# Performance work log

Measured on AMD Instinct MI355X. Metric: run time of the kernel, lower is better.

## Reference

```python
import jax, jax.numpy as jnp
import numpy as np
import math

MODULE_NUM = 256
OUTPUT_DIM = 257
HID = 64          # self.hidden_dim
STEP_DIM = 16
BATCH = 1024
SOS = MODULE_NUM + 1
EOS = MODULE_NUM
MAX_LEN = MODULE_NUM


def setup_inputs() -> dict:
    key = jax.random.key(0)
    ks = jax.random.split(key, 12)
    s = 0.05
    f32 = jnp.float32
    return {
        "step": 100,
        "batch_size": BATCH,
        "token_embed": jax.random.normal(ks[0], (MODULE_NUM + 2, HID), f32) * s,
        "step_table": jax.random.normal(ks[1], (MAX_LEN + 1, STEP_DIM), f32) * s,
        "w_ih_f": jax.random.normal(ks[2], (3 * HID, HID), f32) * s,
        "w_hh_f": jax.random.normal(ks[3], (3 * HID, HID), f32) * s,
        "b_ih_f": jax.random.normal(ks[4], (3 * HID,), f32) * s,
        "b_hh_f": jax.random.normal(ks[5], (3 * HID,), f32) * s,
        "w_ih_b": jax.random.normal(ks[6], (3 * HID, HID), f32) * s,
        "w_hh_b": jax.random.normal(ks[7], (3 * HID, HID), f32) * s,
        "b_ih_b": jax.random.normal(ks[8], (3 * HID,), f32) * s,
        "b_hh_b": jax.random.normal(ks[9], (3 * HID,), f32) * s,
        "film_w": jax.random.normal(ks[10], (4 * HID, STEP_DIM), f32) * s,
        "film_b": jnp.zeros((4 * HID,), f32),
        "dec_w": jax.random.normal(ks[11], (OUTPUT_DIM, 2 * HID), f32) * s,
        "dec_b": jnp.zeros((OUTPUT_DIM,), f32),
    }


def _gru_cell(x, h, w_ih, w_hh, b_ih, b_hh):
    # PyTorch GRU cell math
    gi = x @ w_ih.T + b_ih              # [B, 3H]
    gh = h @ w_hh.T + b_hh              # [B, 3H]
    i_r, i_z, i_n = jnp.split(gi, 3, axis=-1)
    h_r, h_z, h_n = jnp.split(gh, 3, axis=-1)
    r = jax.nn.sigmoid(i_r + h_r)
    z = jax.nn.sigmoid(i_z + h_z)
    n = jnp.tanh(i_n + r * h_n)
    return (1.0 - z) * n + z * h


def reference(step, batch_size, token_embed, step_table,
              w_ih_f, w_hh_f, b_ih_f, b_hh_f,
              w_ih_b, w_hh_b, b_ih_b, b_hh_b,
              film_w, film_b, dec_w, dec_b):
    # exponential-decay temperature (host scalar, matches _exp_decay_tau)
    tau_max, tau_min, half_life = 2.5, 0.2, 3000
    decay = math.log(2.0) / max(1, half_life)
    temperature = max(1e-06, tau_min + (tau_max - tau_min) * math.exp(-decay * max(0, int(step))))
    B = int(batch_size)

    def step_fn(carry, t):
        h_f, h_b, inp, sel, done = carry
        x = token_embed[inp]                              # [B, H]
        h_f2 = _gru_cell(x, h_f, w_ih_f, w_hh_f, b_ih_f, b_hh_f)
        h_b2 = _gru_cell(x, h_b, w_ih_b, w_hh_b, b_ih_b, b_hh_b)
        hs = jnp.concatenate([h_f2, h_b2], axis=-1)       # [B, 2H]
        film = jnp.tanh(step_table[t] @ film_w.T + film_b)  # [4H]
        gamma, beta = jnp.split(film, 2)
        hs = hs * (1.0 + gamma) + beta
        logits = hs @ dec_w.T + dec_b                     # [B, V]
        masked = jnp.where(sel, -jnp.inf, logits) / temperature
        logp = jax.nn.log_softmax(masked, axis=-1)
        action = jnp.argmax(logp, axis=-1)                # greedy (is_val=True)
        lp = jnp.take_along_axis(logp, action[:, None], axis=-1)[:, 0]
        valid = ~done
        done2 = done | (action == EOS)
        sel2 = sel.at[jnp.arange(B), action].set(True)
        return (h_f2, h_b2, action.astype(jnp.int32), sel2, done2), (action.astype(jnp.int32), lp * valid, valid)

    init = (jnp.zeros((B, HID), jnp.float32),
            jnp.zeros((B, HID), jnp.float32),
            jnp.full((B,), SOS, jnp.int32),
            jnp.zeros((B, OUTPUT_DIM), bool),
            jnp.zeros((B,), bool))
    _, (actions, log_probs, valid) = jax.lax.scan(step_fn, init, jnp.arange(MAX_LEN))
    # [B, L] layout; positions after EOS are masked out via `valid`
    return actions.T, log_probs.T, valid.T
```

## Files before the change

### kernel.cpp

```cpp
#include <hip/hip_runtime.h>
#include <cmath>

typedef float v2f __attribute__((ext_vector_type(2)));

#define GI_STRIDE (258*192)
#define FILM_OFF  (2*GI_STRIDE)
#define TOTAL_PRE (FILM_OFF + 256*256)

#define B_TOT   1024
#define L_MAX   256
#define SOS_TOK 257
#define EOS_TOK 256

#define KEEPF(x) asm volatile("" : "+v"(x))

#define PK_LO(acc, w, x) asm("v_pk_fma_f32 %0, %1, %2, %0 op_sel:[0,0,0] op_sel_hi:[1,0,1]" : "+v"(acc) : "v"(w), "v"(x))
#define PK_HI(acc, w, x) asm("v_pk_fma_f32 %0, %1, %2, %0 op_sel:[0,1,0] op_sel_hi:[1,1,1]" : "+v"(acc) : "v"(w), "v"(x))

#define DPPI(old, src, ctrl, rmask) __builtin_amdgcn_update_dpp(old, src, ctrl, rmask, 0xF, false)

#define AMAX_STAGE(ctrl, rmask) do { \
    const int   _vi = __builtin_bit_cast(int, mv); \
    const float _ov = __builtin_bit_cast(float, DPPI(_vi, _vi, ctrl, rmask)); \
    const int   _oi = DPPI(mi, mi, ctrl, rmask); \
    if (_ov > mv || (_ov == mv && _oi < mi)) { mv = _ov; mi = _oi; } \
} while (0)

#define SUM_STAGE(s, ctrl, rmask) do { \
    (s) += __builtin_bit_cast(float, DPPI(0, __builtin_bit_cast(int, (s)), ctrl, rmask)); \
} while (0)

#define AMAX64() do { \
    AMAX_STAGE(0x111, 0xF); AMAX_STAGE(0x112, 0xF); \
    AMAX_STAGE(0x114, 0xF); AMAX_STAGE(0x118, 0xF); \
    AMAX_STAGE(0x142, 0xA); AMAX_STAGE(0x143, 0xC); \
} while (0)
#define SUM64(s) do { \
    SUM_STAGE(s, 0x111, 0xF); SUM_STAGE(s, 0x112, 0xF); \
    SUM_STAGE(s, 0x114, 0xF); SUM_STAGE(s, 0x118, 0xF); \
    SUM_STAGE(s, 0x142, 0xA); SUM_STAGE(s, 0x143, 0xC); \
} while (0)
#define SUM16(s) do { \
    SUM_STAGE(s, 0x111, 0xF); SUM_STAGE(s, 0x112, 0xF); \
    SUM_STAGE(s, 0x114, 0xF); SUM_STAGE(s, 0x118, 0xF); \
} while (0)

__global__ __launch_bounds__(256) void aag_precompute(
    const float* __restrict__ token_embed,
    const float* __restrict__ step_table,
    const float* __restrict__ w_ih_f, const float* __restrict__ b_ih_f,
    const float* __restrict__ w_ih_b, const float* __restrict__ b_ih_b,
    const float* __restrict__ film_w, const float* __restrict__ film_b,
    float* __restrict__ ws)
{
    int idx = blockIdx.x * 256 + threadIdx.x;
    if (idx < FILM_OFF) {
        int m     = idx / GI_STRIDE;
        int rem   = idx - m * GI_STRIDE;
        int token = rem / 192;
        int r     = rem - token * 192;
        const float* wih = (m ? w_ih_b : w_ih_f) + r * 64;
        const float* te  = token_embed + token * 64;
        float acc = (m ? b_ih_b : b_ih_f)[r];
        #pragma unroll 8
        for (int k = 0; k < 64; ++k) acc += te[k] * wih[k];
        ws[idx] = acc;
    } else if (idx < TOTAL_PRE) {
        int q  = idx - FILM_OFF;
        int tt = q >> 8, j = q & 255;
        const float* st = step_table + tt * 16;
        const float* fw = film_w + j * 16;
        float acc = film_b[j];
        #pragma unroll
        for (int s = 0; s < 16; ++s) acc += st[s] * fw[s];
        int pos = (j < 128) ? (2 * j) : (2 * (j - 128) + 1);
        ws[FILM_OFF + tt * 256 + pos] = tanhf(acc);
    }
}

__global__ __launch_bounds__(512)
__attribute__((amdgpu_waves_per_eu(1, 2)))
void aag_decode(
    const int* __restrict__ step_ptr,
    const float* __restrict__ w_hh_f, const float* __restrict__ b_hh_f,
    const float* __restrict__ w_hh_b, const float* __restrict__ b_hh_b,
    const float* __restrict__ dec_w, const float* __restrict__ dec_b,
    const float* __restrict__ ws,
    float* __restrict__ out)
{
    __shared__ __align__(16) float hbuf[2][4][64];
    __shared__ __align__(16) float ghL[2][4][192];
    __shared__ __align__(16) float hsL[4][128];
    __shared__ __align__(16) float plL[2][4][264];

    const int tid = threadIdx.x;
    const int wv  = tid >> 6;
    const int ln  = tid & 63;
    const int e   = wv >> 1;
    const int m   = wv & 1;
    const bool sduty = (wv == 0) || (wv == 3) || (wv == 5) || (wv == 6);

    float invT;
    {
        int step = step_ptr[0];
        if (step < 0) step = 0;
        double T = 0.2 + 2.3 * exp(-(0.6931471805599453 / 3000.0) * (double)step);
        if (T < 1e-6) T = 1e-6;
        invT = (float)(1.0 / T);
    }

    const bool isDec = (tid < 256);
    const bool isEos = (tid >= 256 && tid < 272);
    const bool isGru = (tid >= 320);
    const int  dh    = tid >> 7;
    const int  dq    = tid & 127;
    const int  gj    = tid - 320;
    const int  gm    = (gj >= 96) ? 1 : 0;
    const int  gp    = gj - 96 * gm;
    const int  ec    = tid - 256;

    v2f wreg[64];
    #pragma unroll
    for (int j = 0; j < 64; ++j) wreg[j] = (v2f){0.f, 0.f};
    v2f bias2 = {0.f, 0.f};
    if (isDec) {
        const float* dw = dec_w + (2 * dq) * 128 + dh * 64;
        #pragma unroll
        for (int k = 0; k < 64; ++k) wreg[k] = (v2f){dw[k], dw[128 + k]};
        if (dh == 0) bias2 = (v2f){dec_b[2 * dq], dec_b[2 * dq + 1]};
    } else if (isGru) {
        const float* whh = (gm ? w_hh_b : w_hh_f) + (2 * gp) * 64;
        #pragma unroll
        for (int k = 0; k < 64; ++k) wreg[k] = (v2f){whh[k], whh[64 + k]};
        const float* bhh = (gm ? b_hh_b : b_hh_f) + 2 * gp;
        bias2 = (v2f){bhh[0], bhh[1]};
    } else if (isEos) {
        const float* p = dec_w + 256 * 128 + ec * 8;
        #pragma unroll
        for (int k = 0; k < 4; ++k) wreg[k] = (v2f){p[2 * k], p[2 * k + 1]};
        bias2 = (v2f){dec_b[256], 0.f};
    }
    #pragma unroll
    for (int j = 0; j < 64; ++j) KEEPF(wreg[j]);
    KEEPF(bias2);

    ((float*)hbuf)[tid] = 0.f;
    if (isGru) {
        #pragma unroll
        for (int e2 = 0; e2 < 4; ++e2)
            *(v2f*)&ghL[gm][e2][2 * gp] = bias2;
    }

    bool s0m = false, s1m = false, s2m = false, s3m = false, s4m = false;
    bool done = false;

    const float* filmT = ws + FILM_OFF;
    const float* giT   = ws + m * GI_STRIDE;
    float ga, be;
    {
        const float2 f = *(const float2*)&filmT[(m * 64 + ln) * 2];
        ga = f.x; be = f.y;
    }
    float gi_r, gi_z, gi_n;
    {
        const float* gp2 = giT + SOS_TOK * 192;
        gi_r = gp2[ln]; gi_z = gp2[64 + ln]; gi_n = gp2[128 + ln];
    }

    const int b0 = blockIdx.x * 4;
    float* __restrict__ out_act = out;
    float* __restrict__ out_lp  = out + B_TOT * L_MAX;
    float* __restrict__ out_val = out + 2 * B_TOT * L_MAX;

    __syncthreads();

    for (int t = 0; t <= L_MAX; ++t) {
        #pragma unroll
        for (int j = 0; j < 64; ++j) KEEPF(wreg[j]);

        float hr = 0.f, hz = 0.f, hn = 0.f, hp = 0.f;
        if (t < L_MAX) {
            hr = ghL[m][e][ln];
            hz = ghL[m][e][64 + ln];
            hn = ghL[m][e][128 + ln];
            hp = hbuf[m][e][ln];
        }
        if (t > 0) {
            const float u0 = plL[0][e][ln]       + plL[1][e][ln];
            const float u1 = plL[0][e][64 + ln]  + plL[1][e][64 + ln];
            const float u2 = plL[0][e][128 + ln] + plL[1][e][128 + ln];
            const float u3 = plL[0][e][192 + ln] + plL[1][e][192 + ln];
            float mv = s0m ? -INFINITY : u0;
            int   mi = ln;
            { const float v = s1m ? -INFINITY : u1; if (v > mv) { mv = v; mi = 64 + ln; } }
            { const float v = s2m ? -INFINITY : u2; if (v > mv) { mv = v; mi = 128 + ln; } }
            { const float v = s3m ? -INFINITY : u3; if (v > mv) { mv = v; mi = 192 + ln; } }
            float u4 = 0.f;
            if (ln == 0) {
                u4 = plL[0][e][256];
                const float v = s4m ? -INFINITY : u4;
                if (v > mv) { mv = v; mi = 256; }
            }
            AMAX64();
            const int   a   = __builtin_amdgcn_readlane(mi, 63);
            const float mvU = __builtin_bit_cast(float,
                                __builtin_amdgcn_readlane(__builtin_bit_cast(int, mv), 63));
            {
                const float* gp2 = giT + a * 192;
                gi_r = gp2[ln]; gi_z = gp2[64 + ln]; gi_n = gp2[128 + ln];
            }
            if (sduty) {
                float S = 0.f;
                if (!s0m) S += __expf((u0 - mvU) * invT);
                if (!s1m) S += __expf((u1 - mvU) * invT);
                if (!s2m) S += __expf((u2 - mvU) * invT);
                if (!s3m) S += __expf((u3 - mvU) * invT);
                if (ln == 0 && !s4m) S += __expf((u4 - mvU) * invT);
                SUM64(S);
                const float Su = __builtin_bit_cast(float,
                                    __builtin_amdgcn_readlane(__builtin_bit_cast(int, S), 63));
                if (ln == 0) {
                    const int b = b0 + e;
                    out_act[b * L_MAX + (t - 1)] = (float)a;
                    out_lp [b * L_MAX + (t - 1)] = done ? 0.f : -__logf(Su);
                    out_val[b * L_MAX + (t - 1)] = done ? 0.f : 1.f;
                }
            }
            if (a == EOS_TOK) done = true;
            if ((a & 63) == ln) {
                if (a < 64) s0m = true; else if (a < 128) s1m = true;
                else if (a < 192) s2m = true; else if (a < 256) s3m = true;
                else s4m = true;
            }
        }
        if (t == L_MAX) break;

        {
            const float r  = 1.f / (1.f + expf(-(gi_r + hr)));
            const float z  = 1.f / (1.f + expf(-(gi_z + hz)));
            const float n  = tanhf(gi_n + r * hn);
            const float h2 = (1.f - z) * n + z * hp;
            hbuf[m][e][ln] = h2;
            hsL[e][m * 64 + ln] = h2 * (1.f + ga) + be;
        }
        __syncthreads();

        {
            const int tn = (t + 1 < L_MAX) ? t + 1 : L_MAX - 1;
            const float2 f = *(const float2*)&filmT[tn * 256 + (m * 64 + ln) * 2];
            ga = f.x; be = f.y;
        }
        if (isDec) {
            v2f a0 = bias2, a1 = bias2, a2 = bias2, a3 = bias2;
            const int hb = dh * 64;
            #pragma unroll
            for (int jj = 0; jj < 16; ++jj) {
                const float4 x0 = *(const float4*)&hsL[0][hb + 4 * jj];
                const float4 x1 = *(const float4*)&hsL[1][hb + 4 * jj];
                const float4 x2 = *(const float4*)&hsL[2][hb + 4 * jj];
                const float4 x3 = *(const float4*)&hsL[3][hb + 4 * jj];
                const v2f* x0v = (const v2f*)&x0;
                const v2f* x1v = (const v2f*)&x1;
                const v2f* x2v = (const v2f*)&x2;
                const v2f* x3v = (const v2f*)&x3;
                const v2f w0 = wreg[4*jj], w1 = wreg[4*jj+1], w2 = wreg[4*jj+2], w3 = wreg[4*jj+3];
                PK_LO(a0, w0, x0v[0]); PK_HI(a0, w1, x0v[0]);
                PK_LO(a0, w2, x0v[1]); PK_HI(a0, w3, x0v[1]);
                PK_LO(a1, w0, x1v[0]); PK_HI(a1, w1, x1v[0]);
                PK_LO(a1, w2, x1v[1]); PK_HI(a1, w3, x1v[1]);
                PK_LO(a2, w0, x2v[0]); PK_HI(a2, w1, x2v[0]);
                PK_LO(a2, w2, x2v[1]); PK_HI(a2, w3, x2v[1]);
                PK_LO(a3, w0, x3v[0]); PK_HI(a3, w1, x3v[0]);
                PK_LO(a3, w2, x3v[1]); PK_HI(a3, w3, x3v[1]);
            }
            *(v2f*)&plL[dh][0][2 * dq] = a0;
            *(v2f*)&plL[dh][1][2 * dq] = a1;
            *(v2f*)&plL[dh][2][2 * dq] = a2;
            *(v2f*)&plL[dh][3][2 * dq] = a3;
        } else if (isGru) {
            v2f a0 = bias2, a1 = bias2, a2 = bias2, a3 = bias2;
            #pragma unroll
            for (int jj = 0; jj < 16; ++jj) {
                const float4 x0 = *(const float4*)&hbuf[gm][0][4 * jj];
                const float4 x1 = *(const float4*)&hbuf[gm][1][4 * jj];
                const float4 x2 = *(const float4*)&hbuf[gm][2][4 * jj];
                const float4 x3 = *(const float4*)&hbuf[gm][3][4 * jj];
                const v2f* x0v = (const v2f*)&x0;
                const v2f* x1v = (const v2f*)&x1;
                const v2f* x2v = (const v2f*)&x2;
                const v2f* x3v = (const v2f*)&x3;
                const v2f w0 = wreg[4*jj], w1 = wreg[4*jj+1], w2 = wreg[4*jj+2], w3 = wreg[4*jj+3];
                PK_LO(a0, w0, x0v[0]); PK_HI(a0, w1, x0v[0]);
                PK_LO(a0, w2, x0v[1]); PK_HI(a0, w3, x0v[1]);
                PK_LO(a1, w0, x1v[0]); PK_HI(a1, w1, x1v[0]);
                PK_LO(a1, w2, x1v[1]); PK_HI(a1, w3, x1v[1]);
                PK_LO(a2, w0, x2v[0]); PK_HI(a2, w1, x2v[0]);
                PK_LO(a2, w2, x2v[1]); PK_HI(a2, w3, x2v[1]);
                PK_LO(a3, w0, x3v[0]); PK_HI(a3, w1, x3v[0]);
                PK_LO(a3, w2, x3v[1]); PK_HI(a3, w3, x3v[1]);
            }
            *(v2f*)&ghL[gm][0][2 * gp] = a0;
            *(v2f*)&ghL[gm][1][2 * gp] = a1;
            *(v2f*)&ghL[gm][2][2 * gp] = a2;
            *(v2f*)&ghL[gm][3][2 * gp] = a3;
        } else if (isEos) {
            float t0, t1, t2, t3;
            {
                const float4 p0 = *(const float4*)&hsL[0][8 * ec];
                const float4 p1 = *(const float4*)&hsL[0][8 * ec + 4];
                t0 = p0.x*wreg[0].x + p0.y*wreg[0].y + p0.z*wreg[1].x + p0.w*wreg[1].y
                   + p1.x*wreg[2].x + p1.y*wreg[2].y + p1.z*wreg[3].x + p1.w*wreg[3].y;
            }
            {
                const float4 p0 = *(const float4*)&hsL[1][8 * ec];
                const float4 p1 = *(const float4*)&hsL[1][8 * ec + 4];
                t1 = p0.x*wreg[0].x + p0.y*wreg[0].y + p0.z*wreg[1].x + p0.w*wreg[1].y
                   + p1.x*wreg[2].x + p1.y*wreg[2].y + p1.z*wreg[3].x + p1.w*wreg[3].y;
            }
            {
                const float4 p0 = *(const float4*)&hsL[2][8 * ec];
                const float4 p1 = *(const float4*)&hsL[2][8 * ec + 4];
                t2 = p0.x*wreg[0].x + p0.y*wreg[0].y + p0.z*wreg[1].x + p0.w*wreg[1].y
                   + p1.x*wreg[2].x + p1.y*wreg[2].y + p1.z*wreg[3].x + p1.w*wreg[3].y;
            }
            {
                const float4 p0 = *(const float4*)&hsL[3][8 * ec];
                const float4 p1 = *(const float4*)&hsL[3][8 * ec + 4];
                t3 = p0.x*wreg[0].x + p0.y*wreg[0].y + p0.z*wreg[1].x + p0.w*wreg[1].y
                   + p1.x*wreg[2].x + p1.y*wreg[2].y + p1.z*wreg[3].x + p1.w*wreg[3].y;
            }
            SUM16(t0); SUM16(t1); SUM16(t2); SUM16(t3);
            if (ec == 15) {
                const float dbE = bias2.x;
                plL[0][0][256] = t0 + dbE; plL[0][1][256] = t1 + dbE;
                plL[0][2][256] = t2 + dbE; plL[0][3][256] = t3 + dbE;
            }
        }
        __syncthreads();
    }
}

extern "C" void kernel_launch(void* const* d_in, const int* in_sizes, int n_in,
                              void* d_out, int out_size, void* d_ws, size_t ws_size,
                              hipStream_t stream)
{
    const int*   step        = (const int*)  d_in[0];
    const float* token_embed = (const float*)d_in[2];
    const float* step_table  = (const float*)d_in[3];
    const float* w_ih_f = (const float*)d_in[4];
    const float* w_hh_f = (const float*)d_in[5];
    const float* b_ih_f = (const float*)d_in[6];
    const float* b_hh_f = (const float*)d_in[7];
    const float* w_ih_b = (const float*)d_in[8];
    const float* w_hh_b = (const float*)d_in[9];
    const float* b_ih_b = (const float*)d_in[10];
    const float* b_hh_b = (const float*)d_in[11];
    const float* film_w = (const float*)d_in[12];
    const float* film_b = (const float*)d_in[13];
    const float* dec_w  = (const float*)d_in[14];
    const float* dec_b  = (const float*)d_in[15];
    float* ws   = (float*)d_ws;
    float* outp = (float*)d_out;

    aag_precompute<<<TOTAL_PRE / 256, 256, 0, stream>>>(
        token_embed, step_table, w_ih_f, b_ih_f, w_ih_b, b_ih_b,
        film_w, film_b, ws);
    aag_decode<<<256, 512, 0, stream>>>(
        step, w_hh_f, b_hh_f, w_hh_b, b_hh_b, dec_w, dec_b, ws, outp);
}
```

Baseline: 685.9 us.

## Halve batch rows per block and double grid to 512 blocks

Each decode block now processes 2 batch rows instead of 4, and the grid doubles to 512 blocks. Per-step work per block (GRU recurrent matvec, decoder matvec, EOS logit) is halved, and only half the waves run the gate and argmax phase. The waves_per_eu hint is raised so two blocks can share a CU. The goal is to shorten the serial per-step critical path and use more CUs, at the cost of loading the register-resident weights in twice as many blocks and idling half the waves during the gate phase.

Result: slower. 1.177 ms (+71.5%).

```diff
diff --git a/kernel.cpp b/kernel.cpp
--- a/kernel.cpp
+++ b/kernel.cpp
@@ -79,7 +79,7 @@
 }
 
 __global__ __launch_bounds__(512)
-__attribute__((amdgpu_waves_per_eu(1, 2)))
+__attribute__((amdgpu_waves_per_eu(2, 4)))
 void aag_decode(
     const int* __restrict__ step_ptr,
     const float* __restrict__ w_hh_f, const float* __restrict__ b_hh_f,
@@ -88,17 +88,18 @@
     const float* __restrict__ ws,
     float* __restrict__ out)
 {
-    __shared__ __align__(16) float hbuf[2][4][64];
-    __shared__ __align__(16) float ghL[2][4][192];
-    __shared__ __align__(16) float hsL[4][128];
-    __shared__ __align__(16) float plL[2][4][264];
+    __shared__ __align__(16) float hbuf[2][2][64];
+    __shared__ __align__(16) float ghL[2][2][192];
+    __shared__ __align__(16) float hsL[2][128];
+    __shared__ __align__(16) float plL[2][2][264];
 
     const int tid = threadIdx.x;
     const int wv  = tid >> 6;
     const int ln  = tid & 63;
-    const int e   = wv >> 1;
-    const int m   = wv & 1;
-    const bool sduty = (wv == 0) || (wv == 3) || (wv == 5) || (wv == 6);
+    const int e   = wv >> 2;
+    const int m   = (wv >> 1) & 1;
+    const bool gateW = (wv & 1) == 0;
+    const bool sduty = (wv == 2) || (wv == 4);
 
     float invT;
     {
@@ -144,10 +145,10 @@
     for (int j = 0; j < 64; ++j) KEEPF(wreg[j]);
     KEEPF(bias2);
 
-    ((float*)hbuf)[tid] = 0.f;
+    if (tid < 256) ((float*)hbuf)[tid] = 0.f;
     if (isGru) {
         #pragma unroll
-        for (int e2 = 0; e2 < 4; ++e2)
+        for (int e2 = 0; e2 < 2; ++e2)
             *(v2f*)&ghL[gm][e2][2 * gp] = bias2;
     }
 
@@ -167,7 +168,7 @@
         gi_r = gp2[ln]; gi_z = gp2[64 + ln]; gi_n = gp2[128 + ln];
     }
 
-    const int b0 = blockIdx.x * 4;
+    const int b0 = blockIdx.x * 2;
     float* __restrict__ out_act = out;
     float* __restrict__ out_lp  = out + B_TOT * L_MAX;
     float* __restrict__ out_val = out + 2 * B_TOT * L_MAX;
@@ -179,13 +180,13 @@
         for (int j = 0; j < 64; ++j) KEEPF(wreg[j]);
 
         float hr = 0.f, hz = 0.f, hn = 0.f, hp = 0.f;
-        if (t < L_MAX) {
+        if (gateW && t < L_MAX) {
             hr = ghL[m][e][ln];
             hz = ghL[m][e][64 + ln];
             hn = ghL[m][e][128 + ln];
             hp = hbuf[m][e][ln];
         }
-        if (t > 0) {
+        if (gateW && t > 0) {
             const float u0 = plL[0][e][ln]       + plL[1][e][ln];
             const float u1 = plL[0][e][64 + ln]  + plL[1][e][64 + ln];
             const float u2 = plL[0][e][128 + ln] + plL[1][e][128 + ln];
@@ -235,7 +236,7 @@
         }
         if (t == L_MAX) break;
 
-        {
+        if (gateW) {
             const float r  = 1.f / (1.f + expf(-(gi_r + hr)));
             const float z  = 1.f / (1.f + expf(-(gi_z + hz)));
             const float n  = tanhf(gi_n + r * hn);
@@ -245,66 +246,46 @@
         }
         __syncthreads();
 
-        {
+        if (gateW) {
             const int tn = (t + 1 < L_MAX) ? t + 1 : L_MAX - 1;
             const float2 f = *(const float2*)&filmT[tn * 256 + (m * 64 + ln) * 2];
             ga = f.x; be = f.y;
         }
         if (isDec) {
-            v2f a0 = bias2, a1 = bias2, a2 = bias2, a3 = bias2;
+            v2f a0 = bias2, a1 = bias2;
             const int hb = dh * 64;
             #pragma unroll
             for (int jj = 0; jj < 16; ++jj) {
                 const float4 x0 = *(const float4*)&hsL[0][hb + 4 * jj];
                 const float4 x1 = *(const float4*)&hsL[1][hb + 4 * jj];
-                const float4 x2 = *(const float4*)&hsL[2][hb + 4 * jj];
-                const float4 x3 = *(const float4*)&hsL[3][hb + 4 * jj];
                 const v2f* x0v = (const v2f*)&x0;
                 const v2f* x1v = (const v2f*)&x1;
-                const v2f* x2v = (const v2f*)&x2;
-                const v2f* x3v = (const v2f*)&x3;
                 const v2f w0 = wreg[4*jj], w1 = wreg[4*jj+1], w2 = wreg[4*jj+2], w3 = wreg[4*jj+3];
                 PK_LO(a0, w0, x0v[0]); PK_HI(a0, w1, x0v[0]);
                 PK_LO(a0, w2, x0v[1]); PK_HI(a0, w3, x0v[1]);
                 PK_LO(a1, w0, x1v[0]); PK_HI(a1, w1, x1v[0]);
                 PK_LO(a1, w2, x1v[1]); PK_HI(a1, w3, x1v[1]);
-                PK_LO(a2, w0, x2v[0]); PK_HI(a2, w1, x2v[0]);
-                PK_LO(a2, w2, x2v[1]); PK_HI(a2, w3, x2v[1]);
-                PK_LO(a3, w0, x3v[0]); PK_HI(a3, w1, x3v[0]);
-                PK_LO(a3, w2, x3v[1]); PK_HI(a3, w3, x3v[1]);
             }
             *(v2f*)&plL[dh][0][2 * dq] = a0;
             *(v2f*)&plL[dh][1][2 * dq] = a1;
-            *(v2f*)&plL[dh][2][2 * dq] = a2;
-            *(v2f*)&plL[dh][3][2 * dq] = a3;
         } else if (isGru) {
-            v2f a0 = bias2, a1 = bias2, a2 = bias2, a3 = bias2;
+            v2f a0 = bias2, a1 = bias2;
             #pragma unroll
             for (int jj = 0; jj < 16; ++jj) {
                 const float4 x0 = *(const float4*)&hbuf[gm][0][4 * jj];
                 const float4 x1 = *(const float4*)&hbuf[gm][1][4 * jj];
-                const float4 x2 = *(const float4*)&hbuf[gm][2][4 * jj];
-                const float4 x3 = *(const float4*)&hbuf[gm][3][4 * jj];
                 const v2f* x0v = (const v2f*)&x0;
                 const v2f* x1v = (const v2f*)&x1;
-                const v2f* x2v = (const v2f*)&x2;
-                const v2f* x3v = (const v2f*)&x3;
                 const v2f w0 = wreg[4*jj], w1 = wreg[4*jj+1], w2 = wreg[4*jj+2], w3 = wreg[4*jj+3];
                 PK_LO(a0, w0, x0v[0]); PK_HI(a0, w1, x0v[0]);
                 PK_LO(a0, w2, x0v[1]); PK_HI(a0, w3, x0v[1]);
                 PK_LO(a1, w0, x1v[0]); PK_HI(a1, w1, x1v[0]);
                 PK_LO(a1, w2, x1v[1]); PK_HI(a1, w3, x1v[1]);
-                PK_LO(a2, w0, x2v[0]); PK_HI(a2, w1, x2v[0]);
-                PK_LO(a2, w2, x2v[1]); PK_HI(a2, w3, x2v[1]);
-                PK_LO(a3, w0, x3v[0]); PK_HI(a3, w1, x3v[0]);
-                PK_LO(a3, w2, x3v[1]); PK_HI(a3, w3, x3v[1]);
             }
             *(v2f*)&ghL[gm][0][2 * gp] = a0;
             *(v2f*)&ghL[gm][1][2 * gp] = a1;
-            *(v2f*)&ghL[gm][2][2 * gp] = a2;
-            *(v2f*)&ghL[gm][3][2 * gp] = a3;
         } else if (isEos) {
-            float t0, t1, t2, t3;
+            float t0, t1;
             {
                 const float4 p0 = *(const float4*)&hsL[0][8 * ec];
                 const float4 p1 = *(const float4*)&hsL[0][8 * ec + 4];
@@ -317,23 +298,11 @@
                 t1 = p0.x*wreg[0].x + p0.y*wreg[0].y + p0.z*wreg[1].x + p0.w*wreg[1].y
                    + p1.x*wreg[2].x + p1.y*wreg[2].y + p1.z*wreg[3].x + p1.w*wreg[3].y;
             }
-            {
-                const float4 p0 = *(const float4*)&hsL[2][8 * ec];
-                const float4 p1 = *(const float4*)&hsL[2][8 * ec + 4];
-                t2 = p0.x*wreg[0].x + p0.y*wreg[0].y + p0.z*wreg[1].x + p0.w*wreg[1].y
-                   + p1.x*wreg[2].x + p1.y*wreg[2].y + p1.z*wreg[3].x + p1.w*wreg[3].y;
-            }
-            {
-                const float4 p0 = *(const float4*)&hsL[3][8 * ec];
-                const float4 p1 = *(const float4*)&hsL[3][8 * ec + 4];
-                t3 = p0.x*wreg[0].x + p0.y*wreg[0].y + p0.z*wreg[1].x + p0.w*wreg[1].y
-                   + p1.x*wreg[2].x + p1.y*wreg[2].y + p1.z*wreg[3].x + p1.w*wreg[3].y;
-            }
-            SUM16(t0); SUM16(t1); SUM16(t2); SUM16(t3);
+            SUM16(t0); SUM16(t1);
             if (ec == 15) {
                 const float dbE = bias2.x;
-                plL[0][0][256] = t0 + dbE; plL[0][1][256] = t1 + dbE;
-                plL[0][2][256] = t2 + dbE; plL[0][3][256] = t3 + dbE;
+                plL[0][0][256] = t0 + dbE;
+                plL[0][1][256] = t1 + dbE;
             }
         }
         __syncthreads();
@@ -365,6 +334,6 @@
     aag_precompute<<<TOTAL_PRE / 256, 256, 0, stream>>>(
         token_embed, step_table, w_ih_f, b_ih_f, w_ih_b, b_ih_b,
         film_w, film_b, ws);
-    aag_decode<<<256, 512, 0, stream>>>(
+    aag_decode<<<512, 512, 0, stream>>>(
         step, w_hh_f, b_hh_f, w_hh_b, b_hh_b, dec_w, dec_b, ws, outp);
 }
```
